# Kernel tuning notes

Measured on AMD Instinct MI355X. Metric: run time of the kernel, lower is better.

## Reference

```python
import jax, jax.numpy as jnp
import numpy as np
import math

B, T, D = 2, 2048, 2048
N_HEADS, N_KV_HEADS = 16, 4
HEAD_DIM = D // N_HEADS          # 128
N_GROUPS = N_HEADS // N_KV_HEADS # 4


def setup_inputs() -> dict:
    key = jax.random.key(0)
    k1, k2, k3, k4, k5 = jax.random.split(key, 5)
    x = jax.random.normal(k1, (B, T, D), dtype=jnp.float32)
    # RoPE table: [T, head_dim//2, 2] = (cos, sin)
    inv_freq = 1.0 / (10000.0 ** (np.arange(0, HEAD_DIM, 2, dtype=np.float32) / HEAD_DIM))
    ang = np.arange(T, dtype=np.float32)[:, None] * inv_freq[None, :]  # [T, hd/2]
    rope = jnp.asarray(np.stack([np.cos(ang), np.sin(ang)], axis=-1), dtype=jnp.float32)
    s = 0.02
    wq = s * jax.random.normal(k2, (N_HEADS * HEAD_DIM, D), dtype=jnp.float32)
    wk = s * jax.random.normal(k3, (N_KV_HEADS * HEAD_DIM, D), dtype=jnp.float32)
    wv = s * jax.random.normal(k4, (N_KV_HEADS * HEAD_DIM, D), dtype=jnp.float32)
    wo = s * jax.random.normal(k5, (D, D), dtype=jnp.float32)
    return {"x": x, "rope": rope, "wq": wq, "wk": wk, "wv": wv, "wo": wo}


def apply_rope(t, rope):
    # t: [B, H, T, hd]; rope: [T, hd/2, 2]
    d = t.shape[-1]
    t1, t2 = t[..., : d // 2], t[..., d // 2 :]
    cos = rope[..., 0][None, None]  # [1,1,T,hd/2]
    sin = rope[..., 1][None, None]
    return jnp.concatenate([t1 * cos - t2 * sin, t1 * sin + t2 * cos], axis=-1)


def reference(x, rope, wq, wk, wv, wo):
    b, t, c = x.shape
    q = (x @ wq.T).reshape(b, t, N_HEADS, HEAD_DIM).transpose(0, 2, 1, 3)
    k = (x @ wk.T).reshape(b, t, N_KV_HEADS, HEAD_DIM).transpose(0, 2, 1, 3)
    v = (x @ wv.T).reshape(b, t, N_KV_HEADS, HEAD_DIM).transpose(0, 2, 1, 3)
    q = apply_rope(q, rope)
    k = apply_rope(k, rope)
    k = jnp.repeat(k, N_GROUPS, axis=1)  # [B, H, T, hd]
    v = jnp.repeat(v, N_GROUPS, axis=1)
    scale = 1.0 / math.sqrt(HEAD_DIM)
    scores = jnp.einsum("bhqd,bhkd->bhqk", q, k) * scale
    causal = jnp.tril(jnp.ones((t, t), dtype=bool))
    scores = jnp.where(causal[None, None], scores, jnp.finfo(scores.dtype).min)
    attn = jax.nn.softmax(scores, axis=-1)
    y = jnp.einsum("bhqk,bhkd->bhqd", attn, v)
    y = y.transpose(0, 2, 1, 3).reshape(b, t, c)
    return y @ wo.T
```

## Files before the change

kernel.cpp:

```cpp
#include <hip/hip_runtime.h>

typedef unsigned short u16;
typedef float   f32x4  __attribute__((ext_vector_type(4)));
typedef short   short8 __attribute__((ext_vector_type(8)));
typedef __bf16  bf16x8 __attribute__((ext_vector_type(8)));
typedef float   float4v __attribute__((ext_vector_type(4)));
typedef unsigned short u16x4 __attribute__((ext_vector_type(4)));

static __device__ __forceinline__ u16 f2b(float f) {
  return __builtin_bit_cast(u16, (__bf16)f);
}
static __device__ __forceinline__ float b2f(u16 h) {
  union { unsigned u; float f; } v; v.u = ((unsigned)h) << 16;
  return v.f;
}
static __device__ __forceinline__ f32x4 mfma_bf16(short8 a, short8 b, f32x4 c) {
  return __builtin_amdgcn_mfma_f32_16x16x32_bf16(
      __builtin_bit_cast(bf16x8, a), __builtin_bit_cast(bf16x8, b), c, 0, 0, 0);
}
static __device__ __forceinline__ void gload_lds16(const u16* g, u16* l) {
  __builtin_amdgcn_global_load_lds(
      (const __attribute__((address_space(1))) unsigned int*)g,
      (__attribute__((address_space(3))) unsigned int*)l, 16, 0, 0);
}

#define BB 2
#define TT 2048
#define DD 2048
#define NH 16
#define NKVH 4
#define HD 128
#define MM (BB * TT)
#define QSTR 3072
#define QSCALE 0.08838834764831845f

#define N4_X   ((MM * DD) / 4)
#define N4_WQ  ((DD * DD) / 4)
#define N4_WKV ((NKVH * HD * DD) / 4)
#define N4_WO  ((DD * DD) / 4)
#define N4_TOT (N4_X + N4_WQ + 2 * N4_WKV + N4_WO)

__global__ __launch_bounds__(256) void cvt_all(const float* __restrict__ x,
                                               const float* __restrict__ wq,
                                               const float* __restrict__ wk,
                                               const float* __restrict__ wv,
                                               const float* __restrict__ wo,
                                               u16* __restrict__ xb,
                                               u16* __restrict__ wqkvb,
                                               u16* __restrict__ wob) {
  int stride = gridDim.x * blockDim.x;
  for (int i = blockIdx.x * blockDim.x + threadIdx.x; i < N4_TOT; i += stride) {
    const float4v* src;
    u16x4* dst;
    int off;
    if (i < N4_X) {
      src = (const float4v*)x; dst = (u16x4*)xb; off = i;
    } else if (i < N4_X + N4_WQ) {
      src = (const float4v*)wq; dst = (u16x4*)wqkvb; off = i - N4_X;
    } else if (i < N4_X + N4_WQ + N4_WKV) {
      src = (const float4v*)wk; dst = (u16x4*)wqkvb + N4_WQ; off = i - (N4_X + N4_WQ);
    } else if (i < N4_X + N4_WQ + 2 * N4_WKV) {
      src = (const float4v*)wv; dst = (u16x4*)wqkvb + N4_WQ + N4_WKV;
      off = i - (N4_X + N4_WQ + N4_WKV);
    } else {
      src = (const float4v*)wo; dst = (u16x4*)wob; off = i - (N4_X + N4_WQ + 2 * N4_WKV);
    }
    float4v v = src[off];
    u16x4 o;
    o[0] = f2b(v[0]); o[1] = f2b(v[1]); o[2] = f2b(v[2]); o[3] = f2b(v[3]);
    dst[off] = o;
  }
}

__global__ __launch_bounds__(256) void rope_k(u16* __restrict__ K,
                                              const float* __restrict__ rope) {
  int idx = blockIdx.x * 256 + threadIdx.x;
  int i  = idx & 63;
  int h  = (idx >> 6) & (NKVH - 1);
  int bt = idx >> 8;
  int t  = bt & (TT - 1);
  size_t base = (size_t)bt * QSTR + h * HD + i;
  float x1 = b2f(K[base]);
  float x2 = b2f(K[base + 64]);
  float c = rope[t * 128 + 2 * i];
  float s = rope[t * 128 + 2 * i + 1];
  K[base]      = f2b(x1 * c - x2 * s);
  K[base + 64] = f2b(x1 * s + x2 * c);
}

__global__ __launch_bounds__(512) void gemm_qkv(const u16* __restrict__ A,
                                                const u16* __restrict__ W,
                                                u16* __restrict__ C,
                                                int M, int N, int K) {
  __shared__ __align__(16) u16 As[2][2][128 * 64];
  __shared__ __align__(16) u16 Ws[2][192 * 64];

  const int tid = threadIdx.x, lane = tid & 63, wid = tid >> 6;
  const int wm = wid >> 2, wn = wid & 3;
  const int l15 = lane & 15, lh = lane >> 4;

  const int nwg = gridDim.x * gridDim.y;
  const int lin = blockIdx.y * gridDim.x + blockIdx.x;
  const int swz = (lin & 7) * (nwg >> 3) + (lin >> 3);
  const int brow = (swz / gridDim.x) * 256, bcol = (swz % gridDim.x) * 192;

  const int srp = wid * 8 + (lane >> 3);
  const int gsw = ((lane & 7) ^ (lane >> 3)) << 3;
  const u16* sa[2][2];
  const u16* sw3[3];
#pragma unroll
  for (int mh = 0; mh < 2; ++mh)
#pragma unroll
    for (int i = 0; i < 2; ++i)
      sa[mh][i] = A + (size_t)(brow + mh * 128 + i * 64 + srp) * K + gsw;
#pragma unroll
  for (int i = 0; i < 3; ++i)
    sw3[i] = W + (size_t)(bcol + i * 64 + srp) * K + gsw;

  f32x4 acc[8][3];
#pragma unroll
  for (int mi = 0; mi < 8; ++mi)
#pragma unroll
    for (int ni = 0; ni < 3; ++ni) acc[mi][ni] = (f32x4)0.0f;

  const int nk = K >> 6;

  auto issue = [&](int t, int p) {
#pragma unroll
    for (int mh = 0; mh < 2; ++mh)
#pragma unroll
      for (int i = 0; i < 2; ++i)
        gload_lds16(sa[mh][i] + t * 64, &As[p][mh][i * 4096 + wid * 512]);
#pragma unroll
    for (int i = 0; i < 3; ++i)
      gload_lds16(sw3[i] + t * 64, &Ws[p][i * 4096 + wid * 512]);
  };

  issue(0, 0);
  for (int t = 0; t < nk; ++t) {
    const int p = t & 1;
    if (t + 1 < nk) {
      issue(t + 1, p ^ 1);
      asm volatile("s_waitcnt vmcnt(7)" ::: "memory");
    } else {
      asm volatile("s_waitcnt vmcnt(0)" ::: "memory");
    }
    __builtin_amdgcn_sched_barrier(0);
    __builtin_amdgcn_s_barrier();
    __builtin_amdgcn_sched_barrier(0);

    const u16* Ab = &As[p][wm][0];
    const u16* Wb = &Ws[p][0];

    short8 af[4][2], bf[3][2];
#pragma unroll
    for (int ni = 0; ni < 3; ++ni)
#pragma unroll
      for (int ks = 0; ks < 2; ++ks) {
        int rh = wn * 48 + ni * 16 + l15;
        bf[ni][ks] = *(const short8*)&Wb[rh * 64 + (((ks * 4 + lh) ^ (rh & 7)) << 3)];
      }
#pragma unroll
    for (int mi = 0; mi < 4; ++mi)
#pragma unroll
      for (int ks = 0; ks < 2; ++ks) {
        int rh = mi * 16 + l15;
        af[mi][ks] = *(const short8*)&Ab[rh * 64 + (((ks * 4 + lh) ^ (rh & 7)) << 3)];
      }
    __builtin_amdgcn_s_setprio(1);
#pragma unroll
    for (int mi = 0; mi < 4; ++mi)
#pragma unroll
      for (int ni = 0; ni < 3; ++ni)
#pragma unroll
        for (int ks = 0; ks < 2; ++ks)
          acc[mi][ni] = mfma_bf16(af[mi][ks], bf[ni][ks], acc[mi][ni]);
    __builtin_amdgcn_s_setprio(0);
    __builtin_amdgcn_s_barrier();
#pragma unroll
    for (int mi = 0; mi < 4; ++mi)
#pragma unroll
      for (int ks = 0; ks < 2; ++ks) {
        int rh = (4 + mi) * 16 + l15;
        af[mi][ks] = *(const short8*)&Ab[rh * 64 + (((ks * 4 + lh) ^ (rh & 7)) << 3)];
      }
    __builtin_amdgcn_s_setprio(1);
#pragma unroll
    for (int mi = 0; mi < 4; ++mi)
#pragma unroll
      for (int ni = 0; ni < 3; ++ni)
#pragma unroll
        for (int ks = 0; ks < 2; ++ks)
          acc[4 + mi][ni] = mfma_bf16(af[mi][ks], bf[ni][ks], acc[4 + mi][ni]);
    __builtin_amdgcn_s_setprio(0);

    asm volatile("s_waitcnt lgkmcnt(0)" ::: "memory");
    __builtin_amdgcn_sched_barrier(0);
    __builtin_amdgcn_s_barrier();
    __builtin_amdgcn_sched_barrier(0);
  }

#pragma unroll
  for (int mi = 0; mi < 8; ++mi)
#pragma unroll
    for (int ni = 0; ni < 3; ++ni)
#pragma unroll
      for (int j = 0; j < 4; ++j) {
        int row = brow + wm * 128 + mi * 16 + lh * 4 + j;
        int col = bcol + wn * 48 + ni * 16 + l15;
        C[(size_t)row * N + col] = f2b(acc[mi][ni][j]);
      }
}

__global__ __launch_bounds__(512, 2) void gemm_wo(const u16* __restrict__ A,
                                                  const u16* __restrict__ W,
                                                  float* __restrict__ C,
                                                  int M, int N, int K) {
  __shared__ __align__(16) u16 As[2][2][128 * 64];
  __shared__ __align__(16) u16 Ws[2][128 * 64];

  const int tid = threadIdx.x, lane = tid & 63, wid = tid >> 6;
  const int wm = wid >> 2, wn = wid & 3;
  const int l15 = lane & 15, lh = lane >> 4;

  const int nwg = gridDim.x * gridDim.y;
  const int lin = blockIdx.y * gridDim.x + blockIdx.x;
  const int swz = (lin & 7) * (nwg >> 3) + (lin >> 3);
  const int brow = (swz / gridDim.x) * 256, bcol = (swz % gridDim.x) * 128;

  const int srp = wid * 8 + (lane >> 3);
  const int gsw = ((lane & 7) ^ (lane >> 3)) << 3;
  const u16* sa[2][2];
  const u16* sw2[2];
#pragma unroll
  for (int mh = 0; mh < 2; ++mh)
#pragma unroll
    for (int i = 0; i < 2; ++i)
      sa[mh][i] = A + (size_t)(brow + mh * 128 + i * 64 + srp) * K + gsw;
#pragma unroll
  for (int i = 0; i < 2; ++i)
    sw2[i] = W + (size_t)(bcol + i * 64 + srp) * K + gsw;

  f32x4 acc[8][2];
#pragma unroll
  for (int mi = 0; mi < 8; ++mi)
#pragma unroll
    for (int ni = 0; ni < 2; ++ni) acc[mi][ni] = (f32x4)0.0f;

  const int nk = K >> 6;

  auto issue = [&](int t, int p) {
#pragma unroll
    for (int mh = 0; mh < 2; ++mh)
#pragma unroll
      for (int i = 0; i < 2; ++i)
        gload_lds16(sa[mh][i] + t * 64, &As[p][mh][i * 4096 + wid * 512]);
#pragma unroll
    for (int i = 0; i < 2; ++i)
      gload_lds16(sw2[i] + t * 64, &Ws[p][i * 4096 + wid * 512]);
  };

  issue(0, 0);
  for (int t = 0; t < nk; ++t) {
    const int p = t & 1;
    if (t + 1 < nk) {
      issue(t + 1, p ^ 1);
      asm volatile("s_waitcnt vmcnt(6)" ::: "memory");
    } else {
      asm volatile("s_waitcnt vmcnt(0)" ::: "memory");
    }
    __builtin_amdgcn_sched_barrier(0);
    __builtin_amdgcn_s_barrier();
    __builtin_amdgcn_sched_barrier(0);

    const u16* Ab = &As[p][wm][0];
    const u16* Wb = &Ws[p][0];

    short8 af[4][2], bf[2][2];
#pragma unroll
    for (int ni = 0; ni < 2; ++ni)
#pragma unroll
      for (int ks = 0; ks < 2; ++ks) {
        int rh = wn * 32 + ni * 16 + l15;
        bf[ni][ks] = *(const short8*)&Wb[rh * 64 + (((ks * 4 + lh) ^ (rh & 7)) << 3)];
      }
#pragma unroll
    for (int mi = 0; mi < 4; ++mi)
#pragma unroll
      for (int ks = 0; ks < 2; ++ks) {
        int rh = mi * 16 + l15;
        af[mi][ks] = *(const short8*)&Ab[rh * 64 + (((ks * 4 + lh) ^ (rh & 7)) << 3)];
      }
    __builtin_amdgcn_s_setprio(1);
#pragma unroll
    for (int mi = 0; mi < 4; ++mi)
#pragma unroll
      for (int ni = 0; ni < 2; ++ni)
#pragma unroll
        for (int ks = 0; ks < 2; ++ks)
          acc[mi][ni] = mfma_bf16(af[mi][ks], bf[ni][ks], acc[mi][ni]);
    __builtin_amdgcn_s_setprio(0);
    __builtin_amdgcn_s_barrier();
#pragma unroll
    for (int mi = 0; mi < 4; ++mi)
#pragma unroll
      for (int ks = 0; ks < 2; ++ks) {
        int rh = (4 + mi) * 16 + l15;
        af[mi][ks] = *(const short8*)&Ab[rh * 64 + (((ks * 4 + lh) ^ (rh & 7)) << 3)];
      }
    __builtin_amdgcn_s_setprio(1);
#pragma unroll
    for (int mi = 0; mi < 4; ++mi)
#pragma unroll
      for (int ni = 0; ni < 2; ++ni)
#pragma unroll
        for (int ks = 0; ks < 2; ++ks)
          acc[4 + mi][ni] = mfma_bf16(af[mi][ks], bf[ni][ks], acc[4 + mi][ni]);
    __builtin_amdgcn_s_setprio(0);

    asm volatile("s_waitcnt lgkmcnt(0)" ::: "memory");
    __builtin_amdgcn_sched_barrier(0);
    __builtin_amdgcn_s_barrier();
    __builtin_amdgcn_sched_barrier(0);
  }

#pragma unroll
  for (int mi = 0; mi < 8; ++mi)
#pragma unroll
    for (int ni = 0; ni < 2; ++ni)
#pragma unroll
      for (int j = 0; j < 4; ++j) {
        int row = brow + wm * 128 + mi * 16 + lh * 4 + j;
        int col = bcol + wn * 32 + ni * 16 + l15;
        C[(size_t)row * N + col] = acc[mi][ni][j];
      }
}

#define QBLK 128
#define KVBLK 128

static __device__ __forceinline__ void attn_tile(
    const short8* qa, f32x4* o, float& l, float& m,
    int qrow0, int kv0,
    const u16* Ks, const unsigned* Vt32, u16* myP,
    int l15, int lh) {
  if (kv0 > qrow0 + 15) return;

  f32x4 st[4];
#pragma unroll
  for (int nt = 0; nt < 4; ++nt) st[nt] = (f32x4)0.0f;
  __builtin_amdgcn_s_setprio(1);
#pragma unroll
  for (int nt = 0; nt < 4; ++nt) {
    const u16* krow = &Ks[(nt * 16 + l15) * 136 + (lh << 3)];
#pragma unroll
    for (int kk = 0; kk < 4; ++kk) {
      short8 kb = *(const short8*)(krow + kk * 32);
      st[nt] = mfma_bf16(kb, qa[kk], st[nt]);
    }
  }
  __builtin_amdgcn_s_setprio(0);

  const int kvq = kv0 + lh * 4 - qrow0 - l15;
#pragma unroll
  for (int nt = 0; nt < 4; ++nt)
#pragma unroll
    for (int j = 0; j < 4; ++j)
      if (kvq + nt * 16 + j > 0) st[nt][j] = -1e30f;

  float mt = st[0][0];
#pragma unroll
  for (int nt = 0; nt < 4; ++nt)
#pragma unroll
    for (int j = 0; j < 4; ++j) mt = fmaxf(mt, st[nt][j]);
  mt = fmaxf(mt, __shfl_xor(mt, 16));
  mt = fmaxf(mt, __shfl_xor(mt, 32));

  if (!__all(mt - m <= 8.0f)) {
    float mn = fmaxf(m, mt);
    float a = __expf(m - mn);
    m = mn;
    l *= a;
    float aj[4];
#pragma unroll
    for (int j = 0; j < 4; ++j) aj[j] = __shfl(a, lh * 4 + j);
#pragma unroll
    for (int n = 0; n < 8; ++n)
#pragma unroll
      for (int j = 0; j < 4; ++j) o[n][j] *= aj[j];
  }

  f32x4 p[4];
  float ps = 0.0f;
#pragma unroll
  for (int nt = 0; nt < 4; ++nt) {
#pragma unroll
    for (int j = 0; j < 4; ++j) p[nt][j] = __expf(st[nt][j] - m);
    ps += (p[nt][0] + p[nt][1]) + (p[nt][2] + p[nt][3]);
  }
  l += ps;

  unsigned* P32 = (unsigned*)myP;
  const int pb = l15 * 36 + lh * 2;
#pragma unroll
  for (int nt = 0; nt < 4; ++nt)
#pragma unroll
    for (int jj = 0; jj < 2; ++jj)
      P32[pb + nt * 8 + jj] =
          (unsigned)f2b(p[nt][2 * jj]) | ((unsigned)f2b(p[nt][2 * jj + 1]) << 16);

  __builtin_amdgcn_s_setprio(1);
#pragma unroll
  for (int c = 0; c < 2; ++c) {
    short8 pa = *(const short8*)&myP[l15 * 72 + c * 32 + (lh << 3)];
#pragma unroll
    for (int nt2 = 0; nt2 < 8; ++nt2) {
      int d = nt2 * 16 + l15;
      int byteoff = (d * 144 + (c * 32 + lh * 8) * 2) ^ (((d >> 3) & 7) << 4);
      short8 vb = *(const short8*)((const char*)Vt32 + byteoff);
      o[nt2] = mfma_bf16(pa, vb, o[nt2]);
    }
  }
  __builtin_amdgcn_s_setprio(0);
}

__global__ __launch_bounds__(512) void attn_kernel(const u16* __restrict__ QKV,
                                                   const float* __restrict__ rope,
                                                   u16* __restrict__ Y) {
  __shared__ __align__(16) u16 Ks[2][64 * 136];
  __shared__ __align__(16) unsigned Vt32[2][128 * 36];
  __shared__ __align__(16) u16 Ps[8][16 * 72];

  const int tid = threadIdx.x, lane = tid & 63, wid = tid >> 6;
  const int l15 = lane & 15, lh = lane >> 4;
  const int bid = blockIdx.x;
  const int qpair = bid & 7;
  const int h = (bid >> 3) & 15;
  const int b = bid >> 7;
  const int kvh = h >> 2;
  const int qtA = qpair, qtB = 15 - qpair;
  const int rowA = qtA * QBLK + wid * 16;
  const int rowB = qtB * QBLK + wid * 16;

  const u16* Kb_ = QKV + (size_t)b * TT * QSTR + DD + kvh * HD;
  const u16* Vb_ = Kb_ + NKVH * HD;

  short8 qaA[4], qaB[4];
  {
    const u16* qA = QKV + (size_t)(b * TT + rowA + l15) * QSTR + h * HD + (lh << 3);
    const u16* qB = QKV + (size_t)(b * TT + rowB + l15) * QSTR + h * HD + (lh << 3);
#pragma unroll
    for (int kk = 0; kk < 4; ++kk) {
      qaA[kk] = *(const short8*)(qA + kk * 32);
      qaB[kk] = *(const short8*)(qB + kk * 32);
    }
  }
  {
    const float* rpA = rope + (size_t)(rowA + l15) * 128;
    const float* rpB = rope + (size_t)(rowB + l15) * 128;
#pragma unroll
    for (int kk = 0; kk < 2; ++kk)
#pragma unroll
      for (int e = 0; e < 8; ++e) {
        const int i2 = 2 * (kk * 32 + (lh << 3) + e);
        float c = rpA[i2], s = rpA[i2 + 1];
        float x1 = b2f((u16)qaA[kk][e]), x2 = b2f((u16)qaA[kk + 2][e]);
        qaA[kk][e]     = (short)f2b(QSCALE * (x1 * c - x2 * s));
        qaA[kk + 2][e] = (short)f2b(QSCALE * (x1 * s + x2 * c));
        float cb = rpB[i2], sb = rpB[i2 + 1];
        float y1 = b2f((u16)qaB[kk][e]), y2 = b2f((u16)qaB[kk + 2][e]);
        qaB[kk][e]     = (short)f2b(QSCALE * (y1 * cb - y2 * sb));
        qaB[kk + 2][e] = (short)f2b(QSCALE * (y1 * sb + y2 * cb));
      }
  }

  f32x4 oA[8], oB[8];
  float lA = 0.0f, lB = 0.0f;
  float mA = -1e30f, mB = -1e30f;
#pragma unroll
  for (int n = 0; n < 8; ++n) { oA[n] = (f32x4)0.0f; oB[n] = (f32x4)0.0f; }

  const int kvend = (qtB + 1) * QBLK;

  short8 kreg[4], vreg[4];
  const int srow = tid >> 4;
  const int sc8 = (tid & 15) << 3;

  auto issue = [&](int kv0) {
    kreg[0] = *(const short8*)&Kb_[(size_t)(kv0 + srow) * QSTR + sc8];
    kreg[1] = *(const short8*)&Kb_[(size_t)(kv0 + 32 + srow) * QSTR + sc8];
    kreg[2] = *(const short8*)&Kb_[(size_t)(kv0 + 64 + srow) * QSTR + sc8];
    kreg[3] = *(const short8*)&Kb_[(size_t)(kv0 + 96 + srow) * QSTR + sc8];
    vreg[0] = *(const short8*)&Vb_[(size_t)(kv0 + 2 * srow) * QSTR + sc8];
    vreg[1] = *(const short8*)&Vb_[(size_t)(kv0 + 2 * srow + 1) * QSTR + sc8];
    vreg[2] = *(const short8*)&Vb_[(size_t)(kv0 + 64 + 2 * srow) * QSTR + sc8];
    vreg[3] = *(const short8*)&Vb_[(size_t)(kv0 + 64 + 2 * srow + 1) * QSTR + sc8];
  };

  issue(0);
  for (int kv0 = 0; kv0 < kvend; kv0 += KVBLK) {
    __syncthreads();
    *(short8*)&Ks[0][srow * 136 + sc8] = kreg[0];
    *(short8*)&Ks[0][(srow + 32) * 136 + sc8] = kreg[1];
    *(short8*)&Ks[1][srow * 136 + sc8] = kreg[2];
    *(short8*)&Ks[1][(srow + 32) * 136 + sc8] = kreg[3];
#pragma unroll
    for (int e = 0; e < 8; ++e) {
      int d = sc8 + e;
      unsigned pk0 = (unsigned)(u16)vreg[0][e] | ((unsigned)(u16)vreg[1][e] << 16);
      unsigned pk1 = (unsigned)(u16)vreg[2][e] | ((unsigned)(u16)vreg[3][e] << 16);
      int byteoff = (d * 144 + 4 * srow) ^ (((d >> 3) & 7) << 4);
      *(unsigned*)((char*)&Vt32[0][0] + byteoff) = pk0;
      *(unsigned*)((char*)&Vt32[1][0] + byteoff) = pk1;
    }
    __syncthreads();
    if (kv0 + KVBLK < kvend) issue(kv0 + KVBLK);

    attn_tile(qaA, oA, lA, mA, rowA, kv0,      &Ks[0][0], &Vt32[0][0], &Ps[wid][0], l15, lh);
    attn_tile(qaA, oA, lA, mA, rowA, kv0 + 64, &Ks[1][0], &Vt32[1][0], &Ps[wid][0], l15, lh);
    attn_tile(qaB, oB, lB, mB, rowB, kv0,      &Ks[0][0], &Vt32[0][0], &Ps[wid][0], l15, lh);
    attn_tile(qaB, oB, lB, mB, rowB, kv0 + 64, &Ks[1][0], &Vt32[1][0], &Ps[wid][0], l15, lh);
  }

  lA += __shfl_xor(lA, 16); lA += __shfl_xor(lA, 32);
  lB += __shfl_xor(lB, 16); lB += __shfl_xor(lB, 32);
  f32x4 invA, invB;
#pragma unroll
  for (int j = 0; j < 4; ++j) {
    invA[j] = __builtin_amdgcn_rcpf(__shfl(lA, lh * 4 + j));
    invB[j] = __builtin_amdgcn_rcpf(__shfl(lB, lh * 4 + j));
  }
#pragma unroll
  for (int nt = 0; nt < 8; ++nt)
#pragma unroll
    for (int j = 0; j < 4; ++j) {
      Y[(size_t)(b * TT + rowA + lh * 4 + j) * DD + h * HD + nt * 16 + l15] =
          f2b(oA[nt][j] * invA[j]);
      Y[(size_t)(b * TT + rowB + lh * 4 + j) * DD + h * HD + nt * 16 + l15] =
          f2b(oB[nt][j] * invB[j]);
    }
}

extern "C" void kernel_launch(void* const* d_in, const int* in_sizes, int n_in,
                              void* d_out, int out_size, void* d_ws, size_t ws_size,
                              hipStream_t stream) {
  const float* x    = (const float*)d_in[0];
  const float* rope = (const float*)d_in[1];
  const float* wq   = (const float*)d_in[2];
  const float* wk   = (const float*)d_in[3];
  const float* wv   = (const float*)d_in[4];
  const float* wo   = (const float*)d_in[5];
  float* out = (float*)d_out;

  char* ws = (char*)d_ws;
  u16* xb    = (u16*)ws; ws += (size_t)MM * DD * 2;
  u16* wqkvb = (u16*)ws; ws += (size_t)QSTR * DD * 2;
  u16* wob   = (u16*)ws; ws += (size_t)DD * DD * 2;
  u16* QKVb  = (u16*)ws; ws += (size_t)MM * QSTR * 2;
  u16* Yb    = (u16*)ws;

  cvt_all<<<2048, 256, 0, stream>>>(x, wq, wk, wv, wo, xb, wqkvb, wob);

  gemm_qkv<<<dim3(QSTR / 192, MM / 256), 512, 0, stream>>>(xb, wqkvb, QKVb, MM, QSTR, DD);

  rope_k<<<(MM * NKVH * 64) / 256, 256, 0, stream>>>(QKVb + DD, rope);

  attn_kernel<<<BB * NH * (TT / QBLK / 2), 512, 0, stream>>>(QKVb, rope, Yb);

  gemm_wo<<<dim3(DD / 128, MM / 256), 512, 0, stream>>>(Yb, wob, out, MM, DD, DD);
}
```

Measured before the change: 200.1 us.

## Split attention query tiles across 16 waves instead of two per wave

The attention kernel moves from 512 to 1024 threads per block. Each of 16 waves now owns a single 16-row query strip, from either the low or the high causal tile of the pair. Previously each of 8 waves handled one strip from both tiles in turn. The aim is more waves per CU to hide latency and half the per-wave accumulator and register state. K/V staging is redistributed so each thread loads half as much. The cost is larger per-SIMD register pressure limits and waves on the short causal tile that may sit through extra barrier iterations.

New measurement: 206.2 us. 3.1% more time.

```diff
diff --git a/kernel.cpp b/kernel.cpp
--- a/kernel.cpp
+++ b/kernel.cpp
@@ -424,12 +424,12 @@
   __builtin_amdgcn_s_setprio(0);
 }
 
-__global__ __launch_bounds__(512) void attn_kernel(const u16* __restrict__ QKV,
-                                                   const float* __restrict__ rope,
-                                                   u16* __restrict__ Y) {
+__global__ __launch_bounds__(1024) void attn_kernel(const u16* __restrict__ QKV,
+                                                    const float* __restrict__ rope,
+                                                    u16* __restrict__ Y) {
   __shared__ __align__(16) u16 Ks[2][64 * 136];
   __shared__ __align__(16) unsigned Vt32[2][128 * 36];
-  __shared__ __align__(16) u16 Ps[8][16 * 72];
+  __shared__ __align__(16) u16 Ps[16][16 * 72];
 
   const int tid = threadIdx.x, lane = tid & 63, wid = tid >> 6;
   const int l15 = lane & 15, lh = lane >> 4;
@@ -439,106 +439,81 @@
   const int b = bid >> 7;
   const int kvh = h >> 2;
   const int qtA = qpair, qtB = 15 - qpair;
-  const int rowA = qtA * QBLK + wid * 16;
-  const int rowB = qtB * QBLK + wid * 16;
+  const int myqt = (wid < 8) ? qtA : qtB;
+  const int row0 = myqt * QBLK + (wid & 7) * 16;
 
   const u16* Kb_ = QKV + (size_t)b * TT * QSTR + DD + kvh * HD;
   const u16* Vb_ = Kb_ + NKVH * HD;
 
-  short8 qaA[4], qaB[4];
+  short8 qa[4];
   {
-    const u16* qA = QKV + (size_t)(b * TT + rowA + l15) * QSTR + h * HD + (lh << 3);
-    const u16* qB = QKV + (size_t)(b * TT + rowB + l15) * QSTR + h * HD + (lh << 3);
-#pragma unroll
-    for (int kk = 0; kk < 4; ++kk) {
-      qaA[kk] = *(const short8*)(qA + kk * 32);
-      qaB[kk] = *(const short8*)(qB + kk * 32);
-    }
+    const u16* qp = QKV + (size_t)(b * TT + row0 + l15) * QSTR + h * HD + (lh << 3);
+#pragma unroll
+    for (int kk = 0; kk < 4; ++kk) qa[kk] = *(const short8*)(qp + kk * 32);
   }
   {
-    const float* rpA = rope + (size_t)(rowA + l15) * 128;
-    const float* rpB = rope + (size_t)(rowB + l15) * 128;
+    const float* rp = rope + (size_t)(row0 + l15) * 128;
 #pragma unroll
     for (int kk = 0; kk < 2; ++kk)
 #pragma unroll
       for (int e = 0; e < 8; ++e) {
         const int i2 = 2 * (kk * 32 + (lh << 3) + e);
-        float c = rpA[i2], s = rpA[i2 + 1];
-        float x1 = b2f((u16)qaA[kk][e]), x2 = b2f((u16)qaA[kk + 2][e]);
-        qaA[kk][e]     = (short)f2b(QSCALE * (x1 * c - x2 * s));
-        qaA[kk + 2][e] = (short)f2b(QSCALE * (x1 * s + x2 * c));
-        float cb = rpB[i2], sb = rpB[i2 + 1];
-        float y1 = b2f((u16)qaB[kk][e]), y2 = b2f((u16)qaB[kk + 2][e]);
-        qaB[kk][e]     = (short)f2b(QSCALE * (y1 * cb - y2 * sb));
-        qaB[kk + 2][e] = (short)f2b(QSCALE * (y1 * sb + y2 * cb));
-      }
-  }
-
-  f32x4 oA[8], oB[8];
-  float lA = 0.0f, lB = 0.0f;
-  float mA = -1e30f, mB = -1e30f;
-#pragma unroll
-  for (int n = 0; n < 8; ++n) { oA[n] = (f32x4)0.0f; oB[n] = (f32x4)0.0f; }
+        float c = rp[i2], s = rp[i2 + 1];
+        float x1 = b2f((u16)qa[kk][e]), x2 = b2f((u16)qa[kk + 2][e]);
+        qa[kk][e]     = (short)f2b(QSCALE * (x1 * c - x2 * s));
+        qa[kk + 2][e] = (short)f2b(QSCALE * (x1 * s + x2 * c));
+      }
+  }
+
+  f32x4 o[8];
+  float l = 0.0f, m = -1e30f;
+#pragma unroll
+  for (int n = 0; n < 8; ++n) o[n] = (f32x4)0.0f;
 
   const int kvend = (qtB + 1) * QBLK;
 
-  short8 kreg[4], vreg[4];
+  short8 kreg[2], vreg[2];
   const int srow = tid >> 4;
+  const int sv = srow & 31, ss = srow >> 5;
   const int sc8 = (tid & 15) << 3;
 
   auto issue = [&](int kv0) {
     kreg[0] = *(const short8*)&Kb_[(size_t)(kv0 + srow) * QSTR + sc8];
-    kreg[1] = *(const short8*)&Kb_[(size_t)(kv0 + 32 + srow) * QSTR + sc8];
-    kreg[2] = *(const short8*)&Kb_[(size_t)(kv0 + 64 + srow) * QSTR + sc8];
-    kreg[3] = *(const short8*)&Kb_[(size_t)(kv0 + 96 + srow) * QSTR + sc8];
-    vreg[0] = *(const short8*)&Vb_[(size_t)(kv0 + 2 * srow) * QSTR + sc8];
-    vreg[1] = *(const short8*)&Vb_[(size_t)(kv0 + 2 * srow + 1) * QSTR + sc8];
-    vreg[2] = *(const short8*)&Vb_[(size_t)(kv0 + 64 + 2 * srow) * QSTR + sc8];
-    vreg[3] = *(const short8*)&Vb_[(size_t)(kv0 + 64 + 2 * srow + 1) * QSTR + sc8];
+    kreg[1] = *(const short8*)&Kb_[(size_t)(kv0 + 64 + srow) * QSTR + sc8];
+    vreg[0] = *(const short8*)&Vb_[(size_t)(kv0 + ss * 64 + 2 * sv) * QSTR + sc8];
+    vreg[1] = *(const short8*)&Vb_[(size_t)(kv0 + ss * 64 + 2 * sv + 1) * QSTR + sc8];
   };
 
   issue(0);
   for (int kv0 = 0; kv0 < kvend; kv0 += KVBLK) {
     __syncthreads();
     *(short8*)&Ks[0][srow * 136 + sc8] = kreg[0];
-    *(short8*)&Ks[0][(srow + 32) * 136 + sc8] = kreg[1];
-    *(short8*)&Ks[1][srow * 136 + sc8] = kreg[2];
-    *(short8*)&Ks[1][(srow + 32) * 136 + sc8] = kreg[3];
+    *(short8*)&Ks[1][srow * 136 + sc8] = kreg[1];
 #pragma unroll
     for (int e = 0; e < 8; ++e) {
       int d = sc8 + e;
-      unsigned pk0 = (unsigned)(u16)vreg[0][e] | ((unsigned)(u16)vreg[1][e] << 16);
-      unsigned pk1 = (unsigned)(u16)vreg[2][e] | ((unsigned)(u16)vreg[3][e] << 16);
-      int byteoff = (d * 144 + 4 * srow) ^ (((d >> 3) & 7) << 4);
-      *(unsigned*)((char*)&Vt32[0][0] + byteoff) = pk0;
-      *(unsigned*)((char*)&Vt32[1][0] + byteoff) = pk1;
+      unsigned pack = (unsigned)(u16)vreg[0][e] | ((unsigned)(u16)vreg[1][e] << 16);
+      int byteoff = (d * 144 + 4 * sv) ^ (((d >> 3) & 7) << 4);
+      *(unsigned*)((char*)&Vt32[ss][0] + byteoff) = pack;
     }
     __syncthreads();
     if (kv0 + KVBLK < kvend) issue(kv0 + KVBLK);
 
-    attn_tile(qaA, oA, lA, mA, rowA, kv0,      &Ks[0][0], &Vt32[0][0], &Ps[wid][0], l15, lh);
-    attn_tile(qaA, oA, lA, mA, rowA, kv0 + 64, &Ks[1][0], &Vt32[1][0], &Ps[wid][0], l15, lh);
-    attn_tile(qaB, oB, lB, mB, rowB, kv0,      &Ks[0][0], &Vt32[0][0], &Ps[wid][0], l15, lh);
-    attn_tile(qaB, oB, lB, mB, rowB, kv0 + 64, &Ks[1][0], &Vt32[1][0], &Ps[wid][0], l15, lh);
-  }
-
-  lA += __shfl_xor(lA, 16); lA += __shfl_xor(lA, 32);
-  lB += __shfl_xor(lB, 16); lB += __shfl_xor(lB, 32);
-  f32x4 invA, invB;
-#pragma unroll
-  for (int j = 0; j < 4; ++j) {
-    invA[j] = __builtin_amdgcn_rcpf(__shfl(lA, lh * 4 + j));
-    invB[j] = __builtin_amdgcn_rcpf(__shfl(lB, lh * 4 + j));
-  }
+    attn_tile(qa, o, l, m, row0, kv0,      &Ks[0][0], &Vt32[0][0], &Ps[wid][0], l15, lh);
+    attn_tile(qa, o, l, m, row0, kv0 + 64, &Ks[1][0], &Vt32[1][0], &Ps[wid][0], l15, lh);
+  }
+
+  l += __shfl_xor(l, 16);
+  l += __shfl_xor(l, 32);
+  f32x4 inv;
+#pragma unroll
+  for (int j = 0; j < 4; ++j) inv[j] = __builtin_amdgcn_rcpf(__shfl(l, lh * 4 + j));
 #pragma unroll
   for (int nt = 0; nt < 8; ++nt)
 #pragma unroll
-    for (int j = 0; j < 4; ++j) {
-      Y[(size_t)(b * TT + rowA + lh * 4 + j) * DD + h * HD + nt * 16 + l15] =
-          f2b(oA[nt][j] * invA[j]);
-      Y[(size_t)(b * TT + rowB + lh * 4 + j) * DD + h * HD + nt * 16 + l15] =
-          f2b(oB[nt][j] * invB[j]);
-    }
+    for (int j = 0; j < 4; ++j)
+      Y[(size_t)(b * TT + row0 + lh * 4 + j) * DD + h * HD + nt * 16 + l15] =
+          f2b(o[nt][j] * inv[j]);
 }
 
 extern "C" void kernel_launch(void* const* d_in, const int* in_sizes, int n_in,
@@ -565,7 +540,7 @@
 
   rope_k<<<(MM * NKVH * 64) / 256, 256, 0, stream>>>(QKVb + DD, rope);
 
-  attn_kernel<<<BB * NH * (TT / QBLK / 2), 512, 0, stream>>>(QKVb, rope, Yb);
+  attn_kernel<<<BB * NH * (TT / QBLK / 2), 1024, 0, stream>>>(QKVb, rope, Yb);
 
   gemm_wo<<<dim3(DD / 128, MM / 256), 512, 0, stream>>>(Yb, wob, out, MM, DD, DD);
 }
```
